# Kernel optimization log

Measured on AMD Instinct MI355X. Metric: run time of the kernel, lower is better.

## Reference

```python
import jax, jax.numpy as jnp
import numpy as np
import math

D_MODEL = 768
NUM_HEADS = 12
D_K = D_MODEL // NUM_HEADS
B, S = 4, 2048


def setup_inputs() -> dict:
    key = jax.random.key(0)
    ks = jax.random.split(key, 11)
    s = 1.0 / math.sqrt(D_MODEL)
    inp = {
        "q": jax.random.normal(ks[0], (B, S, D_MODEL), jnp.float32),
        "k": jax.random.normal(ks[1], (B, S, D_MODEL), jnp.float32),
        "v": jax.random.normal(ks[2], (B, S, D_MODEL), jnp.float32),
        "w_q": jax.random.normal(ks[3], (D_MODEL, D_MODEL), jnp.float32) * s,
        "b_q": jax.random.normal(ks[4], (D_MODEL,), jnp.float32) * s,
        "w_k": jax.random.normal(ks[5], (D_MODEL, D_MODEL), jnp.float32) * s,
        "b_k": jax.random.normal(ks[6], (D_MODEL,), jnp.float32) * s,
        "w_v": jax.random.normal(ks[7], (D_MODEL, D_MODEL), jnp.float32) * s,
        "b_v": jax.random.normal(ks[8], (D_MODEL,), jnp.float32) * s,
        "w_o": jax.random.normal(ks[9], (D_MODEL, D_MODEL), jnp.float32) * s,
        "b_o": jax.random.normal(ks[10], (D_MODEL,), jnp.float32) * s,
    }
    return inp


def reference(q, k, v, w_q, b_q, w_k, b_k, w_v, b_v, w_o, b_o):
    b = q.shape[0]
    # Linear projections (torch Linear: x @ W.T + b), reshape to [B,H,S,d_k]
    def proj(x, w, bias):
        y = x @ w.T + bias
        return y.reshape(b, -1, NUM_HEADS, D_K).transpose(0, 2, 1, 3)

    qh = proj(q, w_q, b_q)
    kh = proj(k, w_k, b_k)
    vh = proj(v, w_v, b_v)

    scale = 1.0 / math.sqrt(D_K)
    scores = jnp.einsum("bhqd,bhkd->bhqk", qh, kh) * scale  # [B,H,S,S]
    attn = jax.nn.softmax(scores, axis=-1)
    # dropout is identity in eval mode
    out = jnp.einsum("bhqk,bhkd->bhqd", attn, vh)
    out = out.transpose(0, 2, 1, 3).reshape(b, -1, D_MODEL)
    return out @ w_o.T + b_o
```

## Files before the change

kernel.cpp:

```cpp
#include <hip/hip_runtime.h>

#define DEV __device__ __forceinline__

typedef __attribute__((ext_vector_type(8))) short short8;
typedef __attribute__((ext_vector_type(4))) float f32x4;
typedef unsigned short u16;
typedef unsigned int u32;

DEV f32x4 mfma16(short8 a, short8 b, f32x4 c) {
    return __builtin_amdgcn_mfma_f32_16x16x32_bf16(a, b, c, 0, 0, 0);
}

DEV u16 f2bf(float f) {
    unsigned u = __builtin_bit_cast(unsigned, f);
    u += 0x7fffu + ((u >> 16) & 1u);
    return (u16)(u >> 16);
}

DEV u32 cvt_pk_bf16(float a, float b) {
    u32 r;
    asm("v_cvt_pk_bf16_f32 %0, %1, %2" : "=v"(r) : "v"(a), "v"(b));
    return r;
}

DEV float fexp2_scaled(float xs) {
    int i = (int)xs + 1065055420;
    return __builtin_bit_cast(float, i);
}

DEV void gload16(const void* g, const void* l) {
    __builtin_amdgcn_global_load_lds(
        (const __attribute__((address_space(1))) unsigned int*)g,
        (__attribute__((address_space(3))) unsigned int*)l, 16, 0, 0);
}

template<int N> DEV void waitvm_barrier() {
    asm volatile("s_waitcnt vmcnt(%0)\n\ts_barrier" :: "n"(N) : "memory");
}

DEV short8 lds_frag_swz(const u16* base, int row, int chunk) {
    int sc = chunk ^ (row & 7);
    return *(const short8*)((const char*)base + row * 128 + sc * 16);
}

__global__ __launch_bounds__(256) void prep(
    const float* __restrict__ q, const float* __restrict__ k, const float* __restrict__ v,
    const float* __restrict__ wq, const float* __restrict__ wk,
    const float* __restrict__ wv, const float* __restrict__ wo,
    u16* __restrict__ xq, u16* __restrict__ xk, u16* __restrict__ xv,
    u16* __restrict__ wqB, u16* __restrict__ wkB, u16* __restrict__ wvB,
    u16* __restrict__ woB)
{
    int b = blockIdx.x;
    const float* s;
    u16* d;
    int i;
    if (b < 18432) {
        int t = b / 6144, r = b % 6144;
        s = t == 0 ? q : t == 1 ? k : v;
        d = t == 0 ? xq : t == 1 ? xk : xv;
        i = r * 256 + threadIdx.x;
    } else {
        int t = (b - 18432) / 576, r = (b - 18432) % 576;
        s = t == 0 ? wq : t == 1 ? wk : t == 2 ? wv : wo;
        d = t == 0 ? wqB : t == 1 ? wkB : t == 2 ? wvB : woB;
        i = r * 256 + threadIdx.x;
    }
    float4 vv = ((const float4*)s)[i];
    ((ushort4*)d)[i] = make_ushort4(f2bf(vv.x), f2bf(vv.y), f2bf(vv.z), f2bf(vv.w));
}

template<int MODE>
DEV void gemm_bf16_body(const u16* __restrict__ A_g, const u16* __restrict__ B_g,
                        const float* __restrict__ bias, float scale,
                        u16* __restrict__ outP, float* __restrict__ outF,
                        int mBase, int nBase)
{
    __shared__ u16 AS[128 * 64], BS[128 * 64];

    const int tid = threadIdx.x;
    const int l = tid & 63, wid = tid >> 6;
    const int wy = wid >> 1, wx = wid & 1;
    const int lr = l & 15, lg = l >> 4;

    f32x4 acc[4][4];
    for (int i = 0; i < 4; ++i)
        for (int j = 0; j < 4; ++j) acc[i][j] = (f32x4)0.0f;

    for (int kt = 0; kt < 12; ++kt) {
        if (kt) __syncthreads();
        for (int r = 0; r < 4; ++r) {
            int c = tid + r * 256;
            int row = c >> 3;
            int sc = (c & 7) ^ (row & 7);
            size_t gA = (size_t)(mBase + row) * 768 + kt * 64 + sc * 8;
            size_t gB = (size_t)(nBase + row) * 768 + kt * 64 + sc * 8;
            gload16(A_g + gA, AS + (size_t)(r * 256 + wid * 64) * 8);
            gload16(B_g + gB, BS + (size_t)(r * 256 + wid * 64) * 8);
        }
        __syncthreads();

        short8 bf[4][2];
        for (int nt = 0; nt < 4; ++nt)
            for (int ks = 0; ks < 2; ++ks)
                bf[nt][ks] = lds_frag_swz(BS, wx * 64 + nt * 16 + lr, ks * 4 + lg);
        for (int mt = 0; mt < 4; ++mt) {
            short8 ah[2];
            for (int ks = 0; ks < 2; ++ks)
                ah[ks] = lds_frag_swz(AS, wy * 64 + mt * 16 + lr, ks * 4 + lg);
            for (int nt = 0; nt < 4; ++nt)
                for (int ks = 0; ks < 2; ++ks)
                    acc[mt][nt] = mfma16(ah[ks], bf[nt][ks], acc[mt][nt]);
        }
    }

    for (int mt = 0; mt < 4; ++mt)
        for (int nt = 0; nt < 4; ++nt) {
            int colg = nBase + wx * 64 + nt * 16 + lr;
            for (int r = 0; r < 4; ++r) {
                int rowg = mBase + wy * 64 + mt * 16 + lg * 4 + r;
                float bv = (MODE == 2) ? bias[rowg] : bias[colg];
                float vv = (acc[mt][nt][r] + bv) * scale;
                if constexpr (MODE == 0) {
                    int b = rowg >> 11, s = rowg & 2047;
                    int h = colg >> 6, d = colg & 63;
                    outP[((size_t)(b * 12 + h) * 2048 + s) * 64 + d] = f2bf(vv);
                } else if constexpr (MODE == 1) {
                    outF[(size_t)rowg * 768 + colg] = vv;
                } else {
                    int b = colg >> 11, s = colg & 2047;
                    int h = rowg >> 6, d = rowg & 63;
                    outP[((size_t)(b * 12 + h) * 64 + d) * 2048 + s] = f2bf(vv);
                }
            }
        }
}

__global__ __launch_bounds__(256, 4) void gemm_proj(
    const u16* __restrict__ xq, const u16* __restrict__ xk, const u16* __restrict__ xv,
    const u16* __restrict__ wq, const u16* __restrict__ wk, const u16* __restrict__ wv,
    const float* __restrict__ bq, const float* __restrict__ bk, const float* __restrict__ bv,
    u16* __restrict__ Qpl, u16* __restrict__ Kpl, u16* __restrict__ Vtp)
{
    int z = blockIdx.z;
    if (z < 2) {
        const u16* X = z ? xk : xq;
        const u16* W = z ? wk : wq;
        const float* bias = z ? bk : bq;
        float scale = z ? 1.0f : 0.125f * 1.44269504f * 8388608.0f;
        u16* o = z ? Kpl : Qpl;
        gemm_bf16_body<0>(X, W, bias, scale, o, nullptr, blockIdx.y * 128, blockIdx.x * 128);
    } else {
        gemm_bf16_body<2>(wv, xv, bv, 1.0f, Vtp, nullptr, blockIdx.x * 128, blockIdx.y * 128);
    }
}

__global__ __launch_bounds__(256, 4) void gemm_out(
    const u16* __restrict__ Op, const u16* __restrict__ woB,
    const float* __restrict__ bias, float* __restrict__ outF)
{
    gemm_bf16_body<1>(Op, woB, bias, 1.0f, nullptr, outF,
                      blockIdx.y * 128, blockIdx.x * 128);
}

__global__ __launch_bounds__(512, 4) void attn8(
    const u16* __restrict__ Qp, const u16* __restrict__ Kp,
    const u16* __restrict__ Vtp, u16* __restrict__ Op)
{
    __shared__ u16 Ks[2][64 * 64], Vs[2][64 * 64];
    __shared__ u16 Eh[128][72];

    const int tid = threadIdx.x;
    const int l = tid & 63, wid = tid >> 6;
    const int lr = l & 15, lg = l >> 4;
    const int bh = blockIdx.x, qt = blockIdx.y;

    const size_t qrow = ((size_t)bh * 2048 + qt * 128 + wid * 16 + lr) * 64;
    short8 q_h[2];
    q_h[0] = *(const short8*)(Qp + qrow + lg * 8);
    q_h[1] = *(const short8*)(Qp + qrow + 32 + lg * 8);

    short8 ones;
    for (int j = 0; j < 8; ++j) ones[j] = (short)0x3F80;

    const int srow_ = tid >> 3, sch_ = (tid & 7) ^ (srow_ & 7);

    f32x4 num[4];
    for (int nt = 0; nt < 4; ++nt) num[nt] = (f32x4)0.0f;
    f32x4 denacc = (f32x4)0.0f;

    auto stageK = [&](int kb, int p) {
        size_t g = ((size_t)bh * 2048 + kb * 64 + srow_) * 64 + sch_ * 8;
        gload16(Kp + g, Ks[p] + (size_t)wid * 512);
    };
    auto stageV = [&](int kb, int p) {
        size_t g = ((size_t)bh * 64 + srow_) * 2048 + kb * 64 + sch_ * 8;
        gload16(Vtp + g, Vs[p] + (size_t)wid * 512);
    };

    stageK(0, 0);
    stageV(0, 0);

    for (int kb = 0; kb < 32; ++kb) {
        const int p = kb & 1;
        waitvm_barrier<0>();
        if (kb < 31) {
            stageK(kb + 1, p ^ 1);
            stageV(kb + 1, p ^ 1);
        }

        f32x4 st[4];
        __builtin_amdgcn_s_setprio(1);
        for (int nt = 0; nt < 4; ++nt) {
            st[nt] = (f32x4)0.0f;
            for (int ks = 0; ks < 2; ++ks) {
                short8 kh = lds_frag_swz(Ks[p], nt * 16 + lr, ks * 4 + lg);
                st[nt] = mfma16(kh, q_h[ks], st[nt]);
            }
        }
        __builtin_amdgcn_s_setprio(0);

        for (int nt = 0; nt < 4; ++nt) {
            u32 pk0 = cvt_pk_bf16(fexp2_scaled(st[nt][0]), fexp2_scaled(st[nt][1]));
            u32 pk1 = cvt_pk_bf16(fexp2_scaled(st[nt][2]), fexp2_scaled(st[nt][3]));
            *(u32*)&Eh[wid * 16 + lr][nt * 16 + lg * 4]     = pk0;
            *(u32*)&Eh[wid * 16 + lr][nt * 16 + lg * 4 + 2] = pk1;
        }

        short8 e0 = *(const short8*)&Eh[wid * 16 + lr][lg * 8];
        short8 e1 = *(const short8*)&Eh[wid * 16 + lr][32 + lg * 8];
        __builtin_amdgcn_s_setprio(1);
        denacc = mfma16(e0, ones, denacc);
        denacc = mfma16(e1, ones, denacc);
        for (int nt = 0; nt < 4; ++nt)
            for (int ks = 0; ks < 2; ++ks) {
                short8 vh = lds_frag_swz(Vs[p], nt * 16 + lr, ks * 4 + lg);
                num[nt] = mfma16(ks ? e1 : e0, vh, num[nt]);
            }
        __builtin_amdgcn_s_setprio(0);
    }

    const int b = bh / 12, h = bh % 12;
    float rden[4];
    for (int r = 0; r < 4; ++r) rden[r] = 1.0f / denacc[r];
    for (int nt = 0; nt < 4; ++nt)
        for (int r = 0; r < 4; ++r) {
            int srow = qt * 128 + wid * 16 + lg * 4 + r;
            size_t rowg = (size_t)b * 2048 + srow;
            int col = h * 64 + nt * 16 + lr;
            Op[rowg * 768 + col] = f2bf(num[nt][r] * rden[r]);
        }
}

extern "C" void kernel_launch(void* const* d_in, const int* in_sizes, int n_in,
                              void* d_out, int out_size, void* d_ws, size_t ws_size,
                              hipStream_t stream)
{
    const float* q   = (const float*)d_in[0];
    const float* k   = (const float*)d_in[1];
    const float* v   = (const float*)d_in[2];
    const float* w_q = (const float*)d_in[3];
    const float* b_q = (const float*)d_in[4];
    const float* w_k = (const float*)d_in[5];
    const float* b_k = (const float*)d_in[6];
    const float* w_v = (const float*)d_in[7];
    const float* b_v = (const float*)d_in[8];
    const float* w_o = (const float*)d_in[9];
    const float* b_o = (const float*)d_in[10];
    float* out = (float*)d_out;

    const size_t PL  = (size_t)48 * 2048 * 64;
    const size_t WPL = (size_t)768 * 768;
    u16* base = (u16*)d_ws;
    u16* xqB = base;
    u16* xkB = base + PL;
    u16* xvB = base + 2 * PL;
    u16* Qpl = base + 3 * PL;
    u16* Kpl = base + 4 * PL;
    u16* Vtp = base + 5 * PL;
    u16* OP  = base + 6 * PL;
    u16* W   = base + 7 * PL;
    u16* wqB = W;
    u16* wkB = W + WPL;
    u16* wvB = W + 2 * WPL;
    u16* woB = W + 3 * WPL;

    dim3 bt(256, 1, 1);
    hipLaunchKernelGGL(prep, dim3(20736), bt, 0, stream,
                       q, k, v, w_q, w_k, w_v, w_o,
                       xqB, xkB, xvB, wqB, wkB, wvB, woB);

    hipLaunchKernelGGL(gemm_proj, dim3(6, 64, 3), bt, 0, stream,
                       xqB, xkB, xvB, wqB, wkB, wvB, b_q, b_k, b_v,
                       Qpl, Kpl, Vtp);

    hipLaunchKernelGGL(attn8, dim3(48, 16), dim3(512, 1, 1), 0, stream,
                       Qpl, Kpl, Vtp, OP);

    hipLaunchKernelGGL(gemm_out, dim3(6, 64), bt, 0, stream,
                       OP, woB, b_o, out);
}
```

Before: 159.3 us.

## Halve attention block to 4 waves, each processing 32 query rows

The attention kernel moves from 8 waves with 16 query rows each to 4 waves with 32 query rows each. Every K and V fragment read from LDS now feeds two MFMAs, which halves LDS fragment traffic per unit of work. Each thread also issues two staging loads per tile. In exchange, register pressure roughly doubles for accumulators and Q fragments, and there are fewer waves per block to hide latency. Launch bounds change to 256 threads with 3 blocks per CU.

```diff
diff --git a/kernel.cpp b/kernel.cpp
--- a/kernel.cpp
+++ b/kernel.cpp
@@ -163,7 +163,7 @@
                       blockIdx.y * 128, blockIdx.x * 128);
 }
 
-__global__ __launch_bounds__(512, 4) void attn8(
+__global__ __launch_bounds__(256, 3) void attn4(
     const u16* __restrict__ Qp, const u16* __restrict__ Kp,
     const u16* __restrict__ Vtp, u16* __restrict__ Op)
 {
@@ -175,27 +175,36 @@
     const int lr = l & 15, lg = l >> 4;
     const int bh = blockIdx.x, qt = blockIdx.y;
 
-    const size_t qrow = ((size_t)bh * 2048 + qt * 128 + wid * 16 + lr) * 64;
-    short8 q_h[2];
-    q_h[0] = *(const short8*)(Qp + qrow + lg * 8);
-    q_h[1] = *(const short8*)(Qp + qrow + 32 + lg * 8);
+    short8 q_h[2][2];
+    for (int s = 0; s < 2; ++s) {
+        size_t qrow = ((size_t)bh * 2048 + qt * 128 + wid * 32 + s * 16 + lr) * 64;
+        q_h[s][0] = *(const short8*)(Qp + qrow + lg * 8);
+        q_h[s][1] = *(const short8*)(Qp + qrow + 32 + lg * 8);
+    }
 
     short8 ones;
     for (int j = 0; j < 8; ++j) ones[j] = (short)0x3F80;
 
-    const int srow_ = tid >> 3, sch_ = (tid & 7) ^ (srow_ & 7);
-
-    f32x4 num[4];
-    for (int nt = 0; nt < 4; ++nt) num[nt] = (f32x4)0.0f;
-    f32x4 denacc = (f32x4)0.0f;
+    f32x4 num[2][4];
+    for (int s = 0; s < 2; ++s)
+        for (int nt = 0; nt < 4; ++nt) num[s][nt] = (f32x4)0.0f;
+    f32x4 denacc[2] = {(f32x4)0.0f, (f32x4)0.0f};
 
     auto stageK = [&](int kb, int p) {
-        size_t g = ((size_t)bh * 2048 + kb * 64 + srow_) * 64 + sch_ * 8;
-        gload16(Kp + g, Ks[p] + (size_t)wid * 512);
+        for (int r = 0; r < 2; ++r) {
+            int c = tid + r * 256;
+            int row = c >> 3, sc = (c & 7) ^ (row & 7);
+            size_t g = ((size_t)bh * 2048 + kb * 64 + row) * 64 + sc * 8;
+            gload16(Kp + g, Ks[p] + (size_t)(r * 256 + wid * 64) * 8);
+        }
     };
     auto stageV = [&](int kb, int p) {
-        size_t g = ((size_t)bh * 64 + srow_) * 2048 + kb * 64 + sch_ * 8;
-        gload16(Vtp + g, Vs[p] + (size_t)wid * 512);
+        for (int r = 0; r < 2; ++r) {
+            int c = tid + r * 256;
+            int row = c >> 3, sc = (c & 7) ^ (row & 7);
+            size_t g = ((size_t)bh * 64 + row) * 2048 + kb * 64 + sc * 8;
+            gload16(Vtp + g, Vs[p] + (size_t)(r * 256 + wid * 64) * 8);
+        }
     };
 
     stageK(0, 0);
@@ -209,47 +218,59 @@
             stageV(kb + 1, p ^ 1);
         }
 
-        f32x4 st[4];
+        f32x4 st[2][4];
+        for (int s = 0; s < 2; ++s)
+            for (int nt = 0; nt < 4; ++nt) st[s][nt] = (f32x4)0.0f;
         __builtin_amdgcn_s_setprio(1);
-        for (int nt = 0; nt < 4; ++nt) {
-            st[nt] = (f32x4)0.0f;
+        for (int nt = 0; nt < 4; ++nt)
             for (int ks = 0; ks < 2; ++ks) {
                 short8 kh = lds_frag_swz(Ks[p], nt * 16 + lr, ks * 4 + lg);
-                st[nt] = mfma16(kh, q_h[ks], st[nt]);
-            }
-        }
+                st[0][nt] = mfma16(kh, q_h[0][ks], st[0][nt]);
+                st[1][nt] = mfma16(kh, q_h[1][ks], st[1][nt]);
+            }
         __builtin_amdgcn_s_setprio(0);
 
-        for (int nt = 0; nt < 4; ++nt) {
-            u32 pk0 = cvt_pk_bf16(fexp2_scaled(st[nt][0]), fexp2_scaled(st[nt][1]));
-            u32 pk1 = cvt_pk_bf16(fexp2_scaled(st[nt][2]), fexp2_scaled(st[nt][3]));
-            *(u32*)&Eh[wid * 16 + lr][nt * 16 + lg * 4]     = pk0;
-            *(u32*)&Eh[wid * 16 + lr][nt * 16 + lg * 4 + 2] = pk1;
-        }
-
-        short8 e0 = *(const short8*)&Eh[wid * 16 + lr][lg * 8];
-        short8 e1 = *(const short8*)&Eh[wid * 16 + lr][32 + lg * 8];
+        for (int s = 0; s < 2; ++s)
+            for (int nt = 0; nt < 4; ++nt) {
+                u32 pk0 = cvt_pk_bf16(fexp2_scaled(st[s][nt][0]), fexp2_scaled(st[s][nt][1]));
+                u32 pk1 = cvt_pk_bf16(fexp2_scaled(st[s][nt][2]), fexp2_scaled(st[s][nt][3]));
+                int erow = wid * 32 + s * 16 + lr;
+                *(u32*)&Eh[erow][nt * 16 + lg * 4]     = pk0;
+                *(u32*)&Eh[erow][nt * 16 + lg * 4 + 2] = pk1;
+            }
+
+        short8 e[2][2];
+        for (int s = 0; s < 2; ++s) {
+            int erow = wid * 32 + s * 16 + lr;
+            e[s][0] = *(const short8*)&Eh[erow][lg * 8];
+            e[s][1] = *(const short8*)&Eh[erow][32 + lg * 8];
+        }
         __builtin_amdgcn_s_setprio(1);
-        denacc = mfma16(e0, ones, denacc);
-        denacc = mfma16(e1, ones, denacc);
+        denacc[0] = mfma16(e[0][0], ones, denacc[0]);
+        denacc[0] = mfma16(e[0][1], ones, denacc[0]);
+        denacc[1] = mfma16(e[1][0], ones, denacc[1]);
+        denacc[1] = mfma16(e[1][1], ones, denacc[1]);
         for (int nt = 0; nt < 4; ++nt)
             for (int ks = 0; ks < 2; ++ks) {
                 short8 vh = lds_frag_swz(Vs[p], nt * 16 + lr, ks * 4 + lg);
-                num[nt] = mfma16(ks ? e1 : e0, vh, num[nt]);
+                num[0][nt] = mfma16(e[0][ks], vh, num[0][nt]);
+                num[1][nt] = mfma16(e[1][ks], vh, num[1][nt]);
             }
         __builtin_amdgcn_s_setprio(0);
     }
 
     const int b = bh / 12, h = bh % 12;
-    float rden[4];
-    for (int r = 0; r < 4; ++r) rden[r] = 1.0f / denacc[r];
-    for (int nt = 0; nt < 4; ++nt)
-        for (int r = 0; r < 4; ++r) {
-            int srow = qt * 128 + wid * 16 + lg * 4 + r;
-            size_t rowg = (size_t)b * 2048 + srow;
-            int col = h * 64 + nt * 16 + lr;
-            Op[rowg * 768 + col] = f2bf(num[nt][r] * rden[r]);
-        }
+    for (int s = 0; s < 2; ++s) {
+        float rden[4];
+        for (int r = 0; r < 4; ++r) rden[r] = 1.0f / denacc[s][r];
+        for (int nt = 0; nt < 4; ++nt)
+            for (int r = 0; r < 4; ++r) {
+                int srow = qt * 128 + wid * 32 + s * 16 + lg * 4 + r;
+                size_t rowg = (size_t)b * 2048 + srow;
+                int col = h * 64 + nt * 16 + lr;
+                Op[rowg * 768 + col] = f2bf(num[s][nt][r] * rden[r]);
+            }
+    }
 }
 
 extern "C" void kernel_launch(void* const* d_in, const int* in_sizes, int n_in,
@@ -294,7 +315,7 @@
                        xqB, xkB, xvB, wqB, wkB, wvB, b_q, b_k, b_v,
                        Qpl, Kpl, Vtp);
 
-    hipLaunchKernelGGL(attn8, dim3(48, 16), dim3(512, 1, 1), 0, stream,
+    hipLaunchKernelGGL(attn4, dim3(48, 16), bt, 0, stream,
                        Qpl, Kpl, Vtp, OP);
 
     hipLaunchKernelGGL(gemm_out, dim3(6, 64), bt, 0, stream,
```

New measurement: 156.0 us. 2.1% less time.
